# Kernel optimization log

Measured on AMD Instinct MI355X. Metric: run time of the kernel, lower is better.

The kernel has to match this reference:

```python
import math
import jax, jax.numpy as jnp
import numpy as np

NUM_HEAD = 16


def setup_inputs() -> dict:
    key = jax.random.key(0)
    k1, k2, k3, k4 = jax.random.split(key, 4)
    B, N, E = 64, 577, 1024
    x = jax.random.normal(k1, (B, N, E), dtype=jnp.float32)
    # nn.Linear weights are [out, in]; applied as x @ W.T. Scale like torch init.
    s = 1.0 / math.sqrt(E)
    Wq = jax.random.normal(k2, (E, E), dtype=jnp.float32) * s
    Wk = jax.random.normal(k3, (E, E), dtype=jnp.float32) * s
    Wv = jax.random.normal(k4, (E, E), dtype=jnp.float32) * s
    return {"x": x, "Wq": Wq, "Wk": Wk, "Wv": Wv}


def reference(x, Wq, Wk, Wv):
    B, N, E = x.shape
    H = NUM_HEAD
    D = E // H
    # QKV projections (bias=False), split heads -> [B, H, N, D]
    def proj(W):
        return (x @ W.T).reshape(B, N, H, D).transpose(0, 2, 1, 3)
    q, k, v = proj(Wq), proj(Wk), proj(Wv)
    # scaled dot-product attention (eval mode: dropout_p = 0)
    scale = 1.0 / math.sqrt(D)
    scores = jnp.einsum("bhnd,bhmd->bhnm", q, k) * scale
    probs = jax.nn.softmax(scores, axis=-1)
    out = jnp.einsum("bhnm,bhmd->bhnd", probs, v)
    # merge heads -> [B, N, E]
    return out.transpose(0, 2, 1, 3).reshape(B, N, E)
```

## Files before the change

### kernel.cpp

```cpp
#include <hip/hip_runtime.h>
#include <hip/hip_bf16.h>


typedef __attribute__((ext_vector_type(8))) short s16x8;
typedef __attribute__((ext_vector_type(4))) float f32x4;
typedef __attribute__((ext_vector_type(16))) float f32x16;
typedef __attribute__((ext_vector_type(4))) unsigned int u32x4;
typedef __attribute__((ext_vector_type(2))) unsigned int u32x2;

#define MFMA16(a, b, c) __builtin_amdgcn_mfma_f32_16x16x32_bf16((a), (b), (c), 0, 0, 0)
#define MFMA32(a, b, c) __builtin_amdgcn_mfma_f32_32x32x16_bf16((a), (b), (c), 0, 0, 0)

__device__ __forceinline__ short f2bf(float f) {
    unsigned u = __builtin_bit_cast(unsigned, f);
    u += 0x7FFFu + ((u >> 16) & 1u);
    return (short)(u >> 16);
}

__device__ __forceinline__ unsigned cvtpk(float lo, float hi) {
    unsigned r;
    asm("v_cvt_pk_bf16_f32 %0, %1, %2" : "=v"(r) : "v"(lo), "v"(hi));
    return r;
}

__device__ __forceinline__ void gload_lds16(const void* g, void* l) {
    __builtin_amdgcn_global_load_lds(
        (const __attribute__((address_space(1))) unsigned int*)g,
        (__attribute__((address_space(3))) unsigned int*)l,
        16, 0, 0);
}

__global__ __launch_bounds__(256) void convert_bf16(
    const float* __restrict__ x,
    const float* __restrict__ Wq,
    const float* __restrict__ Wk,
    const float* __restrict__ Wv,
    short* __restrict__ xb,
    short* __restrict__ Wb)
{
    constexpr size_t NX = 37814272u / 8u;
    constexpr size_t NW = 1048576u / 8u;
    constexpr size_t NTOT = NX + 3u * NW;
    size_t stride = (size_t)gridDim.x * blockDim.x;
    for (size_t c = (size_t)blockIdx.x * blockDim.x + threadIdx.x; c < NTOT; c += stride) {
        const float* src;
        short* dst;
        size_t off;
        if (c < NX) { src = x; off = c * 8; dst = xb + off; }
        else {
            size_t cw = c - NX;
            int wsel = (int)(cw / NW);
            src = (wsel == 0) ? Wq : (wsel == 1) ? Wk : Wv;
            off = (cw - (size_t)wsel * NW) * 8;
            dst = Wb + cw * 8;
        }
        float4 a0 = *reinterpret_cast<const float4*>(src + off);
        float4 a1 = *reinterpret_cast<const float4*>(src + off + 4);
        s16x8 v;
        v[0]=f2bf(a0.x); v[1]=f2bf(a0.y); v[2]=f2bf(a0.z); v[3]=f2bf(a0.w);
        v[4]=f2bf(a1.x); v[5]=f2bf(a1.y); v[6]=f2bf(a1.z); v[7]=f2bf(a1.w);
        *reinterpret_cast<s16x8*>(dst) = v;
    }
}

__global__ __launch_bounds__(512, 2) void qkv_gemm3(
    const short* __restrict__ xb,
    const short* __restrict__ Wb,
    short* __restrict__ Qb,
    short* __restrict__ Kb,
    short* __restrict__ Vb)
{
    constexpr int M = 36928;
    constexpr int NT = 12;
    constexpr int NWG = 145 * NT;
    __shared__ char LDS[131072];

    const int t    = threadIdx.x;
    const int lane = t & 63;
    const int w    = t >> 6;
    const int wr   = w >> 2, wc = w & 3;
    const int ml   = lane & 15, zz = lane >> 4;

    int orig = blockIdx.x;
    int xcd  = orig & 7;
    constexpr int QO = NWG / 8, RO = NWG % 8;
    int id = (xcd < RO ? xcd * (QO + 1) : RO * (QO + 1) + (xcd - RO) * QO) + (orig >> 3);
    const int tileM = (id / NT) * 256;
    const int tileN = (id % NT) * 256;

    const char* Ab = (const char*)xb;
    const char* Bb = (const char*)Wb;

    int s_row[2], s_lcol[2], s_arow[2];
    #pragma unroll
    for (int p = 0; p < 2; ++p) {
        int u = p * 512 + t;
        int row = u >> 2;
        int physu = u & 3;
        s_row[p]  = row;
        s_lcol[p] = ((physu ^ ((row >> 1) & 3)) << 4);
        int ar = tileM + row; if (ar > M - 1) ar = M - 1;
        s_arow[p] = ar;
    }

    #define REGOFF(buf_, op_, ks_) ((buf_) * 65536 + (op_) * 32768 + (ks_) * 16384)

    #define STAGE(tt_, op_, ks_, buf_)                                          \
    {   _Pragma("unroll")                                                       \
        for (int p = 0; p < 2; ++p) {                                           \
            int u = p * 512 + t;                                                \
            size_t gb;                                                          \
            if ((op_) == 0) gb = (size_t)s_arow[p] * 2048 + (tt_) * 128 + (ks_) * 64 + s_lcol[p]; \
            else            gb = (size_t)(tileN + s_row[p]) * 2048 + (tt_) * 128 + (ks_) * 64 + s_lcol[p]; \
            gload_lds16((((op_) == 0) ? Ab : Bb) + gb,                          \
                        LDS + REGOFF(buf_, op_, ks_) + u * 16);                 \
        } }

    auto rdA = [&](int buf, int ks, int mf) {
        int row = wr * 128 + mf * 16 + ml;
        int off = REGOFF(buf, 0, ks) + row * 64 + ((zz ^ ((row >> 1) & 3)) << 4);
        return *reinterpret_cast<const s16x8*>(LDS + off);
    };
    auto rdB = [&](int buf, int ks, int nf) {
        int row = wc * 64 + nf * 16 + ml;
        int off = REGOFF(buf, 1, ks) + row * 64 + ((zz ^ ((row >> 1) & 3)) << 4);
        return *reinterpret_cast<const s16x8*>(LDS + off);
    };

    f32x4 acc[8][4] = {};

    STAGE(0, 0, 0, 0); STAGE(0, 1, 0, 0); STAGE(0, 0, 1, 0); STAGE(0, 1, 1, 0);

    for (int tt = 0; tt < 16; ++tt) {
        const int buf = tt & 1, nbuf = buf ^ 1;
        const bool pre = (tt < 15);

        asm volatile("s_waitcnt vmcnt(4)" ::: "memory");
        __builtin_amdgcn_s_barrier();
        __builtin_amdgcn_sched_barrier(0);
        if (pre) STAGE(tt + 1, 0, 0, nbuf);

        s16x8 a[8];
        #pragma unroll
        for (int mf = 0; mf < 8; ++mf) a[mf] = rdA(buf, 0, mf);
        {
            s16x8 b0 = rdB(buf, 0, 0), b1 = rdB(buf, 0, 1);
            __builtin_amdgcn_s_setprio(1);
            #pragma unroll
            for (int mf = 0; mf < 8; ++mf) {
                acc[mf][0] = MFMA16(a[mf], b0, acc[mf][0]);
                acc[mf][1] = MFMA16(a[mf], b1, acc[mf][1]);
            }
            __builtin_amdgcn_s_setprio(0);
        }
        if (pre) STAGE(tt + 1, 1, 0, nbuf);
        {
            s16x8 b2 = rdB(buf, 0, 2), b3 = rdB(buf, 0, 3);
            __builtin_amdgcn_s_setprio(1);
            #pragma unroll
            for (int mf = 0; mf < 8; ++mf) {
                acc[mf][2] = MFMA16(a[mf], b2, acc[mf][2]);
                acc[mf][3] = MFMA16(a[mf], b3, acc[mf][3]);
            }
            __builtin_amdgcn_s_setprio(0);
        }

        if (pre) { asm volatile("s_waitcnt vmcnt(4)" ::: "memory"); }
        else     { asm volatile("s_waitcnt vmcnt(0)" ::: "memory"); }
        __builtin_amdgcn_s_barrier();
        __builtin_amdgcn_sched_barrier(0);
        if (pre) STAGE(tt + 1, 0, 1, nbuf);

        #pragma unroll
        for (int mf = 0; mf < 8; ++mf) a[mf] = rdA(buf, 1, mf);
        {
            s16x8 b0 = rdB(buf, 1, 0), b1 = rdB(buf, 1, 1);
            __builtin_amdgcn_s_setprio(1);
            #pragma unroll
            for (int mf = 0; mf < 8; ++mf) {
                acc[mf][0] = MFMA16(a[mf], b0, acc[mf][0]);
                acc[mf][1] = MFMA16(a[mf], b1, acc[mf][1]);
            }
            __builtin_amdgcn_s_setprio(0);
        }
        if (pre) STAGE(tt + 1, 1, 1, nbuf);
        {
            s16x8 b2 = rdB(buf, 1, 2), b3 = rdB(buf, 1, 3);
            __builtin_amdgcn_s_setprio(1);
            #pragma unroll
            for (int mf = 0; mf < 8; ++mf) {
                acc[mf][2] = MFMA16(a[mf], b2, acc[mf][2]);
                acc[mf][3] = MFMA16(a[mf], b3, acc[mf][3]);
            }
            __builtin_amdgcn_s_setprio(0);
        }
    }

    const int z2 = tileN >> 10;
    short* Ob = (z2 == 0) ? Qb : (z2 == 1) ? Kb : Vb;
    const int cbase = (tileN & 1023) + wc * 64;

    #pragma unroll
    for (int mf = 0; mf < 8; ++mf) {
        #pragma unroll
        for (int j = 0; j < 4; ++j) {
            int row = tileM + wr * 128 + mf * 16 + zz * 4 + j;
            if (row < M) {
                int b = row / 577;
                int n = row - b * 577;
                #pragma unroll
                for (int nf = 0; nf < 4; ++nf) {
                    int cz = cbase + nf * 16 + ml;
                    int h = cz >> 6, dd = cz & 63;
                    Ob[(((size_t)(b * 16 + h)) * 577 + n) * 64 + dd] = f2bf(acc[mf][nf][j]);
                }
            }
        }
    }
    #undef STAGE
    #undef REGOFF
}

__global__ __launch_bounds__(256) void vtrans(
    const short* __restrict__ Vb,
    short* __restrict__ Vt)
{
    __shared__ short lds[64 * 64];
    const int t  = threadIdx.x;
    const int n0 = blockIdx.x * 64;
    const int bh = blockIdx.y;
    const size_t slab  = (size_t)bh * (577 * 64);
    const size_t vslab = (size_t)bh * (64 * 584);

    int r  = t >> 2;
    int d0 = (t & 3) * 16;
    int row = n0 + r; if (row > 576) row = 576;
    const short* src = Vb + slab + (size_t)row * 64 + d0;
    s16x8 v0 = *reinterpret_cast<const s16x8*>(src);
    s16x8 v1 = *reinterpret_cast<const s16x8*>(src + 8);
    #pragma unroll
    for (int j = 0; j < 8; ++j) {
        lds[(d0 + j) * 64 + r]     = v0[j];
        lds[(d0 + 8 + j) * 64 + r] = v1[j];
    }
    __syncthreads();
    #pragma unroll
    for (int p = 0; p < 2; ++p) {
        int u  = p * 256 + t;
        int dd = u >> 3, ns = u & 7;
        int n  = n0 + ns * 8;
        if (n < 584) {
            s16x8 vv = *reinterpret_cast<const s16x8*>(&lds[dd * 64 + ns * 8]);
            *reinterpret_cast<s16x8*>(Vt + vslab + (size_t)dd * 584 + n) = vv;
        }
    }
}

__global__ __launch_bounds__(256, 4) void attn_fwd5(
    const short* __restrict__ Qb,
    const short* __restrict__ Kb,
    const short* __restrict__ Vt,
    float* __restrict__ out)
{
    constexpr int   N    = 577;
    constexpr float CEXP = 0.18033688011112042f;

    __shared__ short K_lds[2][4096];
    __shared__ short V_lds[2][4096];

    const int t     = threadIdx.x;
    const int lane  = t & 63;
    const int w     = t >> 6;
    const int col_q = lane & 31;
    const int hi    = lane >> 5;
    const int hi8   = hi * 8;
    const int c7    = col_q & 7;

    int bd  = blockIdx.x;
    int xx  = bd & 7;
    int r_  = bd >> 3;
    int qt  = r_ % 5;
    int bh  = (r_ / 5) * 8 + xx;
    const int bB = bh >> 4, hH = bh & 15;
    const size_t slab  = (size_t)bh * (N * 64);
    const size_t vslab = (size_t)bh * (64 * 584);

    const int q0 = qt * 128 + w * 32;

    s16x8 qb[4];
    {
        int qr = q0 + col_q; if (qr > N - 1) qr = N - 1;
        const short* qrow = Qb + slab + (size_t)qr * 64 + hi8;
        #pragma unroll
        for (int ks = 0; ks < 4; ++ks)
            qb[ks] = *reinterpret_cast<const s16x8*>(qrow + ks * 16);
    }

    const int sr = t >> 3;
    const int sp = t & 7;

    float m_run = -1e30f, l_run = 0.f;
    f32x16 o0 = {}, o1 = {};

    #pragma unroll
    for (int p = 0; p < 2; ++p) {
        int rr = p * 32 + sr;
        int sl = sp ^ (rr & 7);
        gload_lds16(Kb + slab + (size_t)rr * 64 + sl * 8, &K_lds[0][(rr * 8 + sp) * 8]);
        gload_lds16(Vt + vslab + (size_t)rr * 584 + sl * 8, &V_lds[0][(rr * 8 + sp) * 8]);
    }
    int cur = 0;

    for (int tile = 0; tile < 10; ++tile) {
        const int kv0 = tile * 64;
        __builtin_amdgcn_sched_barrier(0);
        __builtin_amdgcn_s_barrier();
        if (tile < 9) {
            #pragma unroll
            for (int p = 0; p < 2; ++p) {
                int rr = p * 32 + sr;
                int sl = sp ^ (rr & 7);
                gload_lds16(Kb + slab + (size_t)(kv0 + 64 + rr) * 64 + sl * 8,
                            &K_lds[cur ^ 1][(rr * 8 + sp) * 8]);
                gload_lds16(Vt + vslab + (size_t)rr * 584 + (kv0 + 64) + sl * 8,
                            &V_lds[cur ^ 1][(rr * 8 + sp) * 8]);
            }
            asm volatile("s_waitcnt vmcnt(4)" ::: "memory");
        } else {
            asm volatile("s_waitcnt vmcnt(0)" ::: "memory");
        }
        __builtin_amdgcn_sched_barrier(0);

        const short* KL = &K_lds[cur][0];
        const short* VL = &V_lds[cur][0];

        f32x16 s0 = {}, s1 = {};
        __builtin_amdgcn_s_setprio(1);
        #pragma unroll
        for (int ks = 0; ks < 4; ++ks) {
            s16x8 kf0 = *reinterpret_cast<const s16x8*>(
                KL + ((col_q * 8 + ((2*ks + hi) ^ c7)) * 8));
            s0 = MFMA32(kf0, qb[ks], s0);
        }
        #pragma unroll
        for (int ks = 0; ks < 4; ++ks) {
            s16x8 kf1 = *reinterpret_cast<const s16x8*>(
                KL + (((32 + col_q) * 8 + ((2*ks + hi) ^ c7)) * 8));
            s1 = MFMA32(kf1, qb[ks], s1);
        }
        __builtin_amdgcn_s_setprio(0);

        if (kv0 + 64 > N) {
            #pragma unroll
            for (int r = 0; r < 16; ++r) {
                int crow = (r & 3) + 8 * (r >> 2) + 4 * hi;
                if (kv0 + crow > N - 1) s0[r] = -1e30f;
                s1[r] = -1e30f;
            }
        }

        float pm = s0[0];
        #pragma unroll
        for (int r = 1; r < 15; r += 2) pm = fmaxf(fmaxf(pm, s0[r]), s0[r+1]);
        pm = fmaxf(pm, s0[15]);
        #pragma unroll
        for (int r = 0; r < 16; r += 2) pm = fmaxf(fmaxf(pm, s1[r]), s1[r+1]);
        float pmax2 = fmaxf(pm, __shfl_xor(pm, 32));

        bool need = (pmax2 - m_run) * CEXP > 8.f;
        if (__ballot(need)) {
            float mn   = fmaxf(m_run, pmax2);
            float corr = exp2f(CEXP * (m_run - mn));
            m_run = mn;
            l_run *= corr;
            #pragma unroll
            for (int r = 0; r < 16; ++r) { o0[r] *= corr; o1[r] *= corr; }
        }
        float cmn = CEXP * m_run;

        float psum = 0.f;
        #pragma unroll
        for (int r = 0; r < 16; ++r) { s0[r] = exp2f(__builtin_fmaf(s0[r], CEXP, -cmn)); psum += s0[r]; }
        #pragma unroll
        for (int r = 0; r < 16; ++r) { s1[r] = exp2f(__builtin_fmaf(s1[r], CEXP, -cmn)); psum += s1[r]; }
        l_run += psum + __shfl_xor(psum, 32);

        #define REPACK(S_, b_, dst_)                                              \
        {   u32x2 r1_ = __builtin_amdgcn_permlane32_swap(                         \
                cvtpk(S_[(b_)+0], S_[(b_)+1]), cvtpk(S_[(b_)+4], S_[(b_)+5]), false, false); \
            u32x2 r2_ = __builtin_amdgcn_permlane32_swap(                         \
                cvtpk(S_[(b_)+2], S_[(b_)+3]), cvtpk(S_[(b_)+6], S_[(b_)+7]), false, false); \
            dst_[0] = r1_[0]; dst_[2] = r1_[1]; dst_[1] = r2_[0]; dst_[3] = r2_[1]; }

        #define PVSTEP(ks_, S_, b_)                                               \
        {   u32x4 pwk_;                                                           \
            REPACK(S_, b_, pwk_);                                                 \
            s16x8 paf_ = __builtin_bit_cast(s16x8, pwk_);                         \
            s16x8 vf0_ = *reinterpret_cast<const s16x8*>(                         \
                VL + ((col_q * 8 + ((2*(ks_) + hi) ^ c7)) * 8));                  \
            o0 = MFMA32(vf0_, paf_, o0);                                          \
            s16x8 vf1_ = *reinterpret_cast<const s16x8*>(                         \
                VL + (((32 + col_q) * 8 + ((2*(ks_) + hi) ^ c7)) * 8));           \
            o1 = MFMA32(vf1_, paf_, o1);                                          \
        }

        __builtin_amdgcn_s_setprio(1);
        PVSTEP(0, s0, 0)
        PVSTEP(1, s0, 8)
        PVSTEP(2, s1, 0)
        PVSTEP(3, s1, 8)
        __builtin_amdgcn_s_setprio(0);
        #undef PVSTEP
        #undef REPACK
        cur ^= 1;
    }

    int q = q0 + col_q;
    if (q < N) {
        float inv = 1.0f / l_run;
        float* obase = out + ((size_t)bB * 577 + q) * 1024 + (size_t)hH * 64;
        #pragma unroll
        for (int gq = 0; gq < 4; ++gq) {
            float4 v0 = { o0[4*gq+0]*inv, o0[4*gq+1]*inv, o0[4*gq+2]*inv, o0[4*gq+3]*inv };
            *reinterpret_cast<float4*>(obase + 8*gq + 4*hi) = v0;
            float4 v1 = { o1[4*gq+0]*inv, o1[4*gq+1]*inv, o1[4*gq+2]*inv, o1[4*gq+3]*inv };
            *reinterpret_cast<float4*>(obase + 32 + 8*gq + 4*hi) = v1;
        }
    }
}

extern "C" void kernel_launch(void* const* d_in, const int* in_sizes, int n_in,
                              void* d_out, int out_size, void* d_ws, size_t ws_size,
                              hipStream_t stream) {
    const float* x  = (const float*)d_in[0];
    const float* Wq = (const float*)d_in[1];
    const float* Wk = (const float*)d_in[2];
    const float* Wv = (const float*)d_in[3];
    float* out = (float*)d_out;

    const size_t SZ   = (size_t)64 * 16 * 577 * 64 * 2;
    const size_t VTSZ = (size_t)1024 * 64 * 584 * 2;
    short* Qb = (short*)d_ws;
    short* Kb = (short*)((char*)d_ws + SZ);
    short* Vt = (short*)((char*)d_ws + 2 * SZ);
    short* Wb = (short*)((char*)d_ws + 2 * SZ + VTSZ);

    short* xb = (short*)d_out;
    short* Vb = (short*)((char*)d_out + SZ);

    convert_bf16<<<2048, 256, 0, stream>>>(x, Wq, Wk, Wv, xb, Wb);
    qkv_gemm3<<<dim3(145 * 12), 512, 0, stream>>>(xb, Wb, Qb, Kb, Vb);
    vtrans<<<dim3(10, 1024), 256, 0, stream>>>(Vb, Vt);
    attn_fwd5<<<5120, 256, 0, stream>>>(Qb, Kb, Vt, out);
}
```

Baseline: 483.1 us.

## Restructure QKV GEMM main loop into quadrant-wise register double-buffered pipeline

Reorganizes the QKV projection GEMM inner loop to process the accumulator tile in four quadrants, with A/B fragments double-buffered in registers (current/next). LDS reads for the next quadrant and the next k-tile are issued while MFMAs for the current quadrant run, and the global-to-LDS stages are grouped into two issue points per iteration with a single barrier. The aim is to hide LDS latency behind MFMA work and cut barriers per iteration. The cost is more live registers under a 512x2 launch bound and a full vmcnt(0) wait each iteration, which may expose global load latency.

Measured after the change: 499.3 us. +3.4%, slower.

```diff
diff --git a/kernel.cpp b/kernel.cpp
--- a/kernel.cpp
+++ b/kernel.cpp
@@ -63,7 +63,7 @@
     }
 }
 
-__global__ __launch_bounds__(512, 2) void qkv_gemm3(
+__global__ __launch_bounds__(512, 2) void qkv_gemm4(
     const short* __restrict__ xb,
     const short* __restrict__ Wb,
     short* __restrict__ Qb,
@@ -127,73 +127,70 @@
         return *reinterpret_cast<const s16x8*>(LDS + off);
     };
 
+    #define RD_A(dst_, buf_, mb_)                                  \
+    {   _Pragma("unroll")                                          \
+        for (int mf2 = 0; mf2 < 4; ++mf2) {                        \
+            dst_[mf2*2+0] = rdA(buf_, 0, (mb_)+mf2);               \
+            dst_[mf2*2+1] = rdA(buf_, 1, (mb_)+mf2);               \
+        } }
+    #define RD_B(dst_, buf_, nb_)                                  \
+    {   _Pragma("unroll")                                          \
+        for (int nf2 = 0; nf2 < 2; ++nf2) {                        \
+            dst_[nf2*2+0] = rdB(buf_, 0, (nb_)+nf2);               \
+            dst_[nf2*2+1] = rdB(buf_, 1, (nb_)+nf2);               \
+        } }
+
+    #define QMFMA(AF_, BF_, MH_, NH_)                              \
+    {   __builtin_amdgcn_s_setprio(1);                             \
+        _Pragma("unroll")                                          \
+        for (int mf2 = 0; mf2 < 4; ++mf2)                          \
+            _Pragma("unroll")                                      \
+            for (int nf2 = 0; nf2 < 2; ++nf2)                      \
+                acc[(MH_)*4+mf2][(NH_)*2+nf2] =                    \
+                    MFMA16(AF_[mf2*2+0], BF_[nf2*2+0], acc[(MH_)*4+mf2][(NH_)*2+nf2]); \
+        _Pragma("unroll")                                          \
+        for (int mf2 = 0; mf2 < 4; ++mf2)                          \
+            _Pragma("unroll")                                      \
+            for (int nf2 = 0; nf2 < 2; ++nf2)                      \
+                acc[(MH_)*4+mf2][(NH_)*2+nf2] =                    \
+                    MFMA16(AF_[mf2*2+1], BF_[nf2*2+1], acc[(MH_)*4+mf2][(NH_)*2+nf2]); \
+        __builtin_amdgcn_s_setprio(0); }
+
     f32x4 acc[8][4] = {};
+    s16x8 aC[8], aN[8], bC[4], bN[4];
 
     STAGE(0, 0, 0, 0); STAGE(0, 1, 0, 0); STAGE(0, 0, 1, 0); STAGE(0, 1, 1, 0);
+    asm volatile("s_waitcnt vmcnt(0)" ::: "memory");
+    __builtin_amdgcn_s_barrier();
+    __builtin_amdgcn_sched_barrier(0);
+    RD_A(aC, 0, 0);
+    RD_B(bC, 0, 0);
 
     for (int tt = 0; tt < 16; ++tt) {
         const int buf = tt & 1, nbuf = buf ^ 1;
         const bool pre = (tt < 15);
 
-        asm volatile("s_waitcnt vmcnt(4)" ::: "memory");
+        asm volatile("s_waitcnt lgkmcnt(0)" ::: "memory");
+        __builtin_amdgcn_sched_barrier(0);
+        if (pre) { STAGE(tt + 1, 0, 0, nbuf); STAGE(tt + 1, 1, 0, nbuf); }
+        RD_B(bN, buf, 2);
+        RD_A(aN, buf, 4);
+        QMFMA(aC, bC, 0, 0);
+
+        asm volatile("s_waitcnt lgkmcnt(8)" ::: "memory");
+        __builtin_amdgcn_sched_barrier(0);
+        if (pre) { STAGE(tt + 1, 0, 1, nbuf); STAGE(tt + 1, 1, 1, nbuf); }
+        QMFMA(aC, bN, 0, 1);
+
+        asm volatile("s_waitcnt lgkmcnt(0)" ::: "memory");
+        __builtin_amdgcn_sched_barrier(0);
+        QMFMA(aN, bC, 1, 0);
+
+        asm volatile("s_waitcnt vmcnt(0)" ::: "memory");
         __builtin_amdgcn_s_barrier();
         __builtin_amdgcn_sched_barrier(0);
-        if (pre) STAGE(tt + 1, 0, 0, nbuf);
-
-        s16x8 a[8];
-        #pragma unroll
-        for (int mf = 0; mf < 8; ++mf) a[mf] = rdA(buf, 0, mf);
-        {
-            s16x8 b0 = rdB(buf, 0, 0), b1 = rdB(buf, 0, 1);
-            __builtin_amdgcn_s_setprio(1);
-            #pragma unroll
-            for (int mf = 0; mf < 8; ++mf) {
-                acc[mf][0] = MFMA16(a[mf], b0, acc[mf][0]);
-                acc[mf][1] = MFMA16(a[mf], b1, acc[mf][1]);
-            }
-            __builtin_amdgcn_s_setprio(0);
-        }
-        if (pre) STAGE(tt + 1, 1, 0, nbuf);
-        {
-            s16x8 b2 = rdB(buf, 0, 2), b3 = rdB(buf, 0, 3);
-            __builtin_amdgcn_s_setprio(1);
-            #pragma unroll
-            for (int mf = 0; mf < 8; ++mf) {
-                acc[mf][2] = MFMA16(a[mf], b2, acc[mf][2]);
-                acc[mf][3] = MFMA16(a[mf], b3, acc[mf][3]);
-            }
-            __builtin_amdgcn_s_setprio(0);
-        }
-
-        if (pre) { asm volatile("s_waitcnt vmcnt(4)" ::: "memory"); }
-        else     { asm volatile("s_waitcnt vmcnt(0)" ::: "memory"); }
-        __builtin_amdgcn_s_barrier();
-        __builtin_amdgcn_sched_barrier(0);
-        if (pre) STAGE(tt + 1, 0, 1, nbuf);
-
-        #pragma unroll
-        for (int mf = 0; mf < 8; ++mf) a[mf] = rdA(buf, 1, mf);
-        {
-            s16x8 b0 = rdB(buf, 1, 0), b1 = rdB(buf, 1, 1);
-            __builtin_amdgcn_s_setprio(1);
-            #pragma unroll
-            for (int mf = 0; mf < 8; ++mf) {
-                acc[mf][0] = MFMA16(a[mf], b0, acc[mf][0]);
-                acc[mf][1] = MFMA16(a[mf], b1, acc[mf][1]);
-            }
-            __builtin_amdgcn_s_setprio(0);
-        }
-        if (pre) STAGE(tt + 1, 1, 1, nbuf);
-        {
-            s16x8 b2 = rdB(buf, 1, 2), b3 = rdB(buf, 1, 3);
-            __builtin_amdgcn_s_setprio(1);
-            #pragma unroll
-            for (int mf = 0; mf < 8; ++mf) {
-                acc[mf][2] = MFMA16(a[mf], b2, acc[mf][2]);
-                acc[mf][3] = MFMA16(a[mf], b3, acc[mf][3]);
-            }
-            __builtin_amdgcn_s_setprio(0);
-        }
+        if (pre) { RD_A(aC, nbuf, 0); RD_B(bC, nbuf, 0); }
+        QMFMA(aN, bN, 1, 1);
     }
 
     const int z2 = tileN >> 10;
@@ -219,6 +216,9 @@
     }
     #undef STAGE
     #undef REGOFF
+    #undef RD_A
+    #undef RD_B
+    #undef QMFMA
 }
 
 __global__ __launch_bounds__(256) void vtrans(
@@ -449,7 +449,7 @@
     short* Vb = (short*)((char*)d_out + SZ);
 
     convert_bf16<<<2048, 256, 0, stream>>>(x, Wq, Wk, Wv, xb, Wb);
-    qkv_gemm3<<<dim3(145 * 12), 512, 0, stream>>>(xb, Wb, Qb, Kb, Vb);
+    qkv_gemm4<<<dim3(145 * 12), 512, 0, stream>>>(xb, Wb, Qb, Kb, Vb);
     vtrans<<<dim3(10, 1024), 256, 0, stream>>>(Vb, Vt);
     attn_fwd5<<<5120, 256, 0, stream>>>(Qb, Kb, Vt, out);
 }
```
